# Performance work log

Hardware: AMD Instinct MI355X
Metric: run time of the kernel (lower is better)

The kernel has to match this reference:

```python
import jax, jax.numpy as jnp
import numpy as np
from jax import lax

K = 15            # k_neighbors
EPS = 1e-8
N, D = 8192, 512


def _knn(emb, k):
    # pairwise euclidean distances via gram trick (torch.cdist p=2 equivalent)
    sq = jnp.sum(emb * emb, axis=1)                      # [N]
    d2 = sq[:, None] + sq[None, :] - 2.0 * (emb @ emb.T)  # [N, N]
    d = jnp.where(d2 > 0, jnp.sqrt(jnp.maximum(d2, 1e-24)), 0.0)
    neg_d, idx = lax.top_k(-d, k + 1)                    # smallest k+1 (incl. self)
    return -neg_d[:, 1:], idx[:, 1:]                     # drop self: [N,k], [N,k]


def _local_density(knn_dists):
    return 1.0 / (knn_dists.mean(axis=1) + EPS)          # [N]


def _angular_signature(emb, knn_idx, k):
    nb = emb[knn_idx]                                    # [N, k, D] gather
    v = nb - emb[:, None, :]                             # [N, k, D]
    v = v / jnp.maximum(jnp.linalg.norm(v, axis=2, keepdims=True), 1e-12)
    cos = jnp.einsum('nkd,nld->nkl', v, v)               # [N, k, k]
    iu0, iu1 = np.triu_indices(k, 1)                     # static upper-triangle mask
    return cos[:, iu0, iu1]                              # [N, k*(k-1)/2]


def setup_inputs() -> dict:
    key = jax.random.key(0)
    k1, k2 = jax.random.split(key)
    embeddings = jax.random.normal(k1, (N, D), dtype=jnp.float32)
    ref_embeddings = jax.random.normal(k2, (N, D), dtype=jnp.float32)
    return {"embeddings": embeddings, "ref_embeddings": ref_embeddings}


def reference(embeddings, ref_embeddings):
    k = K
    # reference geometry is a detached buffer (set_reference under no_grad)
    ref = lax.stop_gradient(ref_embeddings)
    ref_dists, ref_idx = _knn(ref, k)
    ref_density = _local_density(ref_dists)
    ref_angular = _angular_signature(ref, ref_idx, k)

    curr_dists, curr_idx = _knn(embeddings, k)

    # 1) normalized distance-distribution loss
    curr_dn = curr_dists / (curr_dists.mean(axis=1, keepdims=True) + EPS)
    ref_dn = ref_dists / (ref_dists.mean(axis=1, keepdims=True) + EPS)
    total = jnp.mean((curr_dn - ref_dn) ** 2)

    # 2) density preservation loss (use_density=True)
    curr_density = _local_density(curr_dists)
    cden = curr_density / (curr_density.mean() + EPS)
    rden = ref_density / (ref_density.mean() + EPS)
    total = total + 0.5 * jnp.mean((cden - rden) ** 2)

    # 3) angular structure loss (use_angular=True)
    curr_angular = _angular_signature(embeddings, curr_idx, k)
    total = total + 0.5 * jnp.mean((curr_angular - ref_angular) ** 2)
    return total
```

## Files before the change

kernel.cpp:

```cpp
#include <hip/hip_runtime.h>

#define N 8192
#define D 512
#define KNN 15
#define SC 8
#define NC 16
#define SPLITS 8
#define NCAND 32
#define NPAIR 105
#define EPSF 1e-8f

#define INF __int_as_float(0x7f800000)

typedef __attribute__((ext_vector_type(4))) float f32x4;
typedef __attribute__((ext_vector_type(4))) unsigned u32x4;
typedef __attribute__((ext_vector_type(8))) short s16x8;
typedef __attribute__((ext_vector_type(8))) unsigned short u16x8;
typedef unsigned long long u64;

typedef const unsigned int __attribute__((address_space(1)))* gp_t;
typedef unsigned int __attribute__((address_space(3)))* lp_t;

__device__ __forceinline__ void gl_lds16(const void* g, void* l) {
  __builtin_amdgcn_global_load_lds((gp_t)g, (lp_t)l, 16, 0, 0);
}

__device__ __forceinline__ unsigned short bf16_rne(float x) {
  unsigned int u = __float_as_uint(x);
  return (unsigned short)((u + 0x7fffu + ((u >> 16) & 1u)) >> 16);
}

#define VMCNT4 asm volatile("s_waitcnt vmcnt(4)" ::: "memory")
#define VMCNT0 asm volatile("s_waitcnt vmcnt(0)" ::: "memory")
#define LGKM0  asm volatile("s_waitcnt lgkmcnt(0)" ::: "memory")
#define CFENCE asm volatile("" ::: "memory")

__global__ __launch_bounds__(256)
void k_prep(const float* __restrict__ A, const float* __restrict__ B,
            unsigned short* __restrict__ hi, float* __restrict__ sq)
{
  const int tid = threadIdx.x;
  const int lane = tid & 63;
  const int row = blockIdx.x * 4 + (tid >> 6);
  const float* src = (row < N) ? (A + (size_t)row * D)
                               : (B + (size_t)(row - N) * D);
  const float4* s4 = (const float4*)src + lane * 2;
  const float4 x0 = s4[0], x1 = s4[1];
  const float xs[8] = {x0.x, x0.y, x0.z, x0.w, x1.x, x1.y, x1.z, x1.w};
  u16x8 hv;
  float s = 0.f;
#pragma unroll
  for (int j = 0; j < 8; ++j) {
    hv[j] = bf16_rne(xs[j]);
    s = fmaf(xs[j], xs[j], s);
  }
  *(u16x8*)(hi + (size_t)row * D + lane * 8) = hv;
#pragma unroll
  for (int o = 32; o; o >>= 1) s += __shfl_xor(s, o);
  if (lane == 0) sq[row] = s;
}

__global__ __launch_bounds__(256, 4)
void k_knn1(const unsigned short* __restrict__ hi,
            const float* __restrict__ sqall,
            unsigned* __restrict__ pk)
{
  __shared__ __align__(16) char smem[40960];
  unsigned* DtU = (unsigned*)smem;
  unsigned* SK = (unsigned*)smem;

  const int tid = threadIdx.x;
  const int lane = tid & 63, w = tid >> 6;
  const int wr = w >> 1, wc = w & 1;
  const int fr = lane & 15, fq = lane >> 4;
  const int sgx = fq ^ ((fr >> 1) & 3);

  const int rb = blockIdx.x, split = blockIdx.y, which = blockIdx.z;
  const int row0 = rb * 128;
  const int c0 = split * 1024;
  const unsigned short* Hi = hi + (size_t)which * N * D;
  const float* sq = sqall + which * N;

  const int rr = tid >> 2, sseg = tid & 3;
  const int ssg = sseg ^ ((rr >> 1) & 3);
  const unsigned short* pAh = Hi + (size_t)(row0 + rr) * D + ssg * 8;
  const unsigned short* pBh = Hi + (size_t)(c0 + rr) * D + ssg * 8;

  auto stage = [&](int sel) {
    char* d = smem + (sel << 14) + (w << 10);
    gl_lds16(pAh, d);
    gl_lds16(pAh + 32768, d + 4096);
    gl_lds16(pBh, d + 8192);
    gl_lds16(pBh + 32768, d + 12288);
    pAh += 32; pBh += 32;
  };

  const int srow = tid >> 1, ssub = tid & 1;
  unsigned tv[SC];
#pragma unroll
  for (int j = 0; j < SC; ++j) tv[j] = 0xFFFFFFFFu;

  float sqr[4][4];
#pragma unroll
  for (int m = 0; m < 4; ++m)
#pragma unroll
    for (int j = 0; j < 4; ++j)
      sqr[m][j] = sq[row0 + wr * 64 + m * 16 + fq * 4 + j];

#pragma unroll 1
  for (int t = 0; t < 8; ++t) {
    const int ct = c0 + t * 128;
    float sqc[4];
#pragma unroll
    for (int n = 0; n < 4; ++n) sqc[n] = sq[ct + wc * 64 + n * 16 + fr];

    f32x4 acc[4][4];
#pragma unroll
    for (int m = 0; m < 4; ++m)
#pragma unroll
      for (int n = 0; n < 4; ++n) acc[m][n] = (f32x4){0.f, 0.f, 0.f, 0.f};

    stage(0);
    int cur = 0;
#pragma unroll 1
    for (int kt = 0; kt < 16; ++kt) {
      if (kt < 15) {
        stage(cur ^ 1);
        VMCNT4;
      } else {
        VMCNT0;
      }
      __builtin_amdgcn_s_barrier();
      CFENCE;

      const short* Sb = (const short*)(smem + (cur << 14));
      s16x8 ah[4], bh[4];
#pragma unroll
      for (int m = 0; m < 4; ++m)
        ah[m] = *(const s16x8*)(Sb + (wr * 64 + m * 16 + fr) * 32 + sgx * 8);
#pragma unroll
      for (int n = 0; n < 4; ++n)
        bh[n] = *(const s16x8*)(Sb + 4096 + (wc * 64 + n * 16 + fr) * 32 + sgx * 8);
#pragma unroll
      for (int m = 0; m < 4; ++m)
#pragma unroll
        for (int n = 0; n < 4; ++n)
          acc[m][n] = __builtin_amdgcn_mfma_f32_16x16x32_bf16(ah[m], bh[n], acc[m][n], 0, 0, 0);

      LGKM0;
      __builtin_amdgcn_s_barrier();
      CFENCE;
      cur ^= 1;
    }
    pAh -= 512; pBh += 65024;

#pragma unroll 1
    for (int h = 0; h < 2; ++h) {
      if (wc == h) {
#pragma unroll
        for (int m = 0; m < 4; ++m)
#pragma unroll
          for (int n = 0; n < 4; ++n) {
            const int cl = n * 16 + fr;
            const int gcol = ct + h * 64 + cl;
            const int rbase = wr * 64 + m * 16 + fq * 4;
#pragma unroll
            for (int j = 0; j < 4; ++j) {
              const float d2 = fmaf(-2.0f, acc[m][n][j], sqr[m][j] + sqc[n]);
              unsigned key = (__float_as_uint(fmaxf(d2, 0.f)) & ~8191u) | (unsigned)gcol;
              if (row0 + rbase + j == gcol) key = 0xFFFFFFFFu;
              DtU[(rbase + j) * 68 + cl] = key;
            }
          }
      }
      __syncthreads();
      {
        unsigned kth = tv[SC - 1];
#pragma unroll 1
        for (int g = 0; g < 8; ++g) {
          const u32x4 dv = *(const u32x4*)&DtU[srow * 68 + ssub * 32 + g * 4];
#pragma unroll
          for (int i = 0; i < 4; ++i) {
            unsigned key = dv[i];
            if (key < kth) {
#pragma unroll
              for (int j = 0; j < SC; ++j) {
                const unsigned lo = min(tv[j], key);
                key = max(tv[j], key);
                tv[j] = lo;
              }
              kth = tv[SC - 1];
            }
          }
        }
      }
      __syncthreads();
    }
  }

#pragma unroll
  for (int j = 0; j < SC; ++j) SK[srow * 16 + ssub * 8 + j] = tv[j];
  __syncthreads();
  if (tid < 128) {
    const int grow = row0 + tid;
    const size_t pb = (((size_t)which * SPLITS + split) * N + grow) * NC;
    int p0 = 0, p1 = 0;
#pragma unroll
    for (int j = 0; j < NC; ++j) {
      const unsigned a = (p0 < SC) ? SK[tid * 16 + p0] : 0xFFFFFFFFu;
      const unsigned b = (p1 < SC) ? SK[tid * 16 + 8 + p1] : 0xFFFFFFFFu;
      const bool ta = a <= b;
      pk[pb + j] = ta ? a : b;
      if (ta) ++p0; else ++p1;
    }
  }
}

__global__ __launch_bounds__(256)
void k_tail(const float* __restrict__ emb, const float* __restrict__ ref,
            const float* __restrict__ sqall, const unsigned* __restrict__ pk,
            float* __restrict__ dens, float* __restrict__ l1p,
            float* __restrict__ angp)
{
  __shared__ __align__(16) short Vb[16][520];
  __shared__ float Gp[4][256];
  __shared__ float G[256];
  __shared__ float invn[16];
  __shared__ float cref[NPAIR];
  __shared__ float red2[256];
  __shared__ int idxs[2][16];
  __shared__ float dls[2][16];

  const int i = blockIdx.x;
  const int tid = threadIdx.x;
  const int lane = tid & 63;
  const int w = tid >> 6;

  if (w < 2) {
    const int which = 1 - w;
    const float* E = which ? ref : emb;
    const float* sqm = sqall + which * N;

    const int sp = lane >> 3, jj = lane & 7;
    const size_t kb = (((size_t)which * SPLITS + sp) * N + i) * NC;
    unsigned v0 = pk[kb + jj];
    unsigned v1 = pk[kb + 8 + jj];

#pragma unroll
    for (int k = 2; k <= 128; k <<= 1) {
#pragma unroll
      for (int s = k >> 1; s > 0; s >>= 1) {
        if (s == 64) {
          const unsigned mn = min(v0, v1), mx = max(v0, v1);
          v0 = mn; v1 = mx;
        } else {
          const unsigned o0 = __shfl_xor(v0, s);
          const unsigned o1 = __shfl_xor(v1, s);
          const bool low = ((lane & s) == 0);
          const bool dir0 = ((lane & k) == 0);
          const bool dir1 = (((64 + lane) & k) == 0);
          const unsigned a0 = min(v0, o0), b0 = max(v0, o0);
          v0 = (low == dir0) ? a0 : b0;
          const unsigned a1 = min(v1, o1), b1 = max(v1, o1);
          v1 = (low == dir1) ? a1 : b1;
        }
      }
    }

    const float4* orow = (const float4*)(E + (size_t)i * D) + lane * 2;
    const float4 o0 = orow[0], o1 = orow[1];
    const float sqr_ = sqm[i];

    u64 mykey = ~0ull;
#pragma unroll 4
    for (int c = 0; c < NCAND; ++c) {
      const int cl = (int)(__shfl(v0, c) & 8191u);
      const float4* crow = (const float4*)(E + (size_t)cl * D) + lane * 2;
      const float4 c0 = crow[0], c1 = crow[1];
      float s = o0.x*c0.x + o0.y*c0.y + o0.z*c0.z + o0.w*c0.w
              + o1.x*c1.x + o1.y*c1.y + o1.z*c1.z + o1.w*c1.w;
#pragma unroll
      for (int o = 32; o; o >>= 1) s += __shfl_xor(s, o);
      float d2 = fmaf(-2.0f, s, sqr_ + sqm[cl]);
      d2 = fmaxf(d2, 0.0f);
      const u64 key = ((u64)__float_as_uint(d2) << 32) | (unsigned)cl;
      if (lane == c) mykey = key;
    }

#pragma unroll
    for (int k = 2; k <= 64; k <<= 1) {
#pragma unroll
      for (int j = k >> 1; j > 0; j >>= 1) {
        const u64 o = __shfl_xor(mykey, j);
        const bool up = ((lane & k) == 0);
        const bool lower = ((lane & j) == 0);
        const u64 mn = (mykey < o) ? mykey : o;
        const u64 mx = (mykey < o) ? o : mykey;
        mykey = (lower == up) ? mn : mx;
      }
    }

    if (lane < KNN) {
      const float d2v = __uint_as_float((unsigned)(mykey >> 32));
      dls[w][lane] = (d2v > 0.f) ? sqrtf(fmaxf(d2v, 1e-24f)) : 0.f;
      idxs[w][lane] = (int)(mykey & 0xffffffffu);
    }
  }
  __syncthreads();

  if (tid == 0) {
    float mr = 0.f, mc = 0.f;
#pragma unroll
    for (int j = 0; j < KNN; ++j) { mr += dls[0][j]; mc += dls[1][j]; }
    mr *= (1.0f / KNN); mc *= (1.0f / KNN);
    const float ir = 1.0f / (mr + EPSF);
    const float ic = 1.0f / (mc + EPSF);
    float s1 = 0.f;
#pragma unroll
    for (int j = 0; j < KNN; ++j) {
      const float t = dls[1][j] * ic - dls[0][j] * ir;
      s1 = fmaf(t, t, s1);
    }
    dens[i] = ic;
    dens[N + i] = ir;
    l1p[i] = s1;
  }
  __syncthreads();

  const int base = lane * 8;
  float acc = 0.f;

#pragma unroll 1
  for (int pass = 0; pass < 2; ++pass) {
    const float* E = pass ? emb : ref;

    const float4* er = (const float4*)(E + (size_t)i * D) + lane * 2;
    const float4 e0 = er[0], e1 = er[1];

#pragma unroll 1
    for (int j = w; j < 16; j += 4) {
      u16x8 hv;
      if (j < 15) {
        const float* src = E + (size_t)idxs[pass][j] * D;
        const float4 x0 = *(const float4*)(src + base);
        const float4 x1 = *(const float4*)(src + base + 4);
        const float dd[8] = {x0.x-e0.x, x0.y-e0.y, x0.z-e0.z, x0.w-e0.w,
                             x1.x-e1.x, x1.y-e1.y, x1.z-e1.z, x1.w-e1.w};
#pragma unroll
        for (int q = 0; q < 8; ++q) hv[q] = bf16_rne(dd[q]);
      } else {
#pragma unroll
        for (int q = 0; q < 8; ++q) hv[q] = 0;
      }
      *(u16x8*)&Vb[j][base] = hv;
    }
    __syncthreads();

    {
      const int r = lane & 15, fq = lane >> 4;
      f32x4 g = (f32x4){0.f, 0.f, 0.f, 0.f};
#pragma unroll
      for (int s = 0; s < 4; ++s) {
        const s16x8 f = *(const s16x8*)&Vb[r][w * 128 + s * 32 + fq * 8];
        g = __builtin_amdgcn_mfma_f32_16x16x32_bf16(f, f, g, 0, 0, 0);
      }
#pragma unroll
      for (int r2 = 0; r2 < 4; ++r2)
        Gp[w][(fq * 4 + r2) * 16 + r] = g[r2];
    }
    __syncthreads();

    G[tid] = Gp[0][tid] + Gp[1][tid] + Gp[2][tid] + Gp[3][tid];
    __syncthreads();
    if (tid < 16) invn[tid] = 1.0f / fmaxf(sqrtf(G[tid * 17]), 1e-12f);
    __syncthreads();

    if (tid < NPAIR) {
      int a = 0, q = tid, rem = KNN - 1;
      while (q >= rem) { q -= rem; ++a; --rem; }
      const int b = a + 1 + q;
      const float cosv = G[a * 16 + b] * invn[a] * invn[b];
      if (pass == 0) cref[tid] = cosv;
      else { const float dd = cosv - cref[tid]; acc = dd * dd; }
    }
    __syncthreads();
  }

  red2[tid] = acc;
  __syncthreads();
  for (int o = 128; o; o >>= 1) {
    if (tid < o) red2[tid] += red2[tid + o];
    __syncthreads();
  }
  if (tid == 0) angp[i] = red2[0];
}

__global__ __launch_bounds__(256)
void k_final(const float* __restrict__ l1p, const float* __restrict__ dens,
             const float* __restrict__ angp, float* __restrict__ out)
{
  __shared__ float red[256];
  const int t = threadIdx.x;

  float sc = 0.f, sr = 0.f;
  for (int n = t; n < N; n += 256) { sc += dens[n]; sr += dens[N + n]; }
  red[t] = sc; __syncthreads();
  for (int o = 128; o; o >>= 1) { if (t < o) red[t] += red[t + o]; __syncthreads(); }
  float scm = red[0]; __syncthreads();
  red[t] = sr; __syncthreads();
  for (int o = 128; o; o >>= 1) { if (t < o) red[t] += red[t + o]; __syncthreads(); }
  float srm = red[0]; __syncthreads();

  const float icm = 1.0f / (scm / (float)N + EPSF);
  const float irm = 1.0f / (srm / (float)N + EPSF);

  float l2 = 0.f;
  for (int n = t; n < N; n += 256) {
    const float dd = dens[n] * icm - dens[N + n] * irm;
    l2 = fmaf(dd, dd, l2);
  }
  red[t] = l2; __syncthreads();
  for (int o = 128; o; o >>= 1) { if (t < o) red[t] += red[t + o]; __syncthreads(); }
  const float l2sum = red[0]; __syncthreads();

  float l1 = 0.f;
  for (int n = t; n < N; n += 256) l1 += l1p[n];
  red[t] = l1; __syncthreads();
  for (int o = 128; o; o >>= 1) { if (t < o) red[t] += red[t + o]; __syncthreads(); }
  const float l1sum = red[0]; __syncthreads();

  float l3 = 0.f;
  for (int n = t; n < N; n += 256) l3 += angp[n];
  red[t] = l3; __syncthreads();
  for (int o = 128; o; o >>= 1) { if (t < o) red[t] += red[t + o]; __syncthreads(); }
  const float l3sum = red[0];

  if (t == 0) {
    out[0] = l1sum / (float)(N * KNN)
           + 0.5f * l2sum / (float)N
           + 0.5f * l3sum / (float)(N * NPAIR);
  }
}

extern "C" void kernel_launch(void* const* d_in, const int* in_sizes, int n_in,
                              void* d_out, int out_size, void* d_ws, size_t ws_size,
                              hipStream_t stream)
{
  const float* emb = (const float*)d_in[0];
  const float* ref = (const float*)d_in[1];
  float* out = (float*)d_out;
  char* ws = (char*)d_ws;

  const size_t off_sq   = 0;
  const size_t off_hi   = off_sq + (size_t)2 * N * 4;
  const size_t off_pk   = off_hi + (size_t)2 * N * D * 2;
  const size_t off_dens = off_pk + (size_t)2 * SPLITS * N * NC * 4;
  const size_t off_l1   = off_dens + (size_t)2 * N * 4;
  const size_t off_ang  = off_l1 + (size_t)N * 4;

  float* sq = (float*)(ws + off_sq);
  unsigned short* hi = (unsigned short*)(ws + off_hi);
  unsigned* pk = (unsigned*)(ws + off_pk);
  float* dens = (float*)(ws + off_dens);
  float* l1p = (float*)(ws + off_l1);
  float* angp = (float*)(ws + off_ang);

  k_prep<<<(2 * N) / 4, 256, 0, stream>>>(emb, ref, hi, sq);
  k_knn1<<<dim3(N / 128, SPLITS, 2), 256, 0, stream>>>(hi, sq, pk);
  k_tail<<<N, 256, 0, stream>>>(emb, ref, sq, pk, dens, l1p, angp);
  k_final<<<1, 256, 0, stream>>>(l1p, dens, angp, out);
}
```

Baseline: 367.2 us.

## Spread candidate rescoring and angular Gram work across all four waves

Candidate rescoring used to run on two waves, one per embedding set, with 32 candidates each. It now uses all four waves at 16 candidates each, sharing candidates and keys through LDS plus extra barriers. The two-pass angular Gram computation becomes a single pass: two waves build each set's difference matrix, and each wave runs 8 MFMAs over half of D. This removes a serial loop and several syncs, in exchange for more LDS and extra barriers around the merge.

```diff
diff --git a/kernel.cpp b/kernel.cpp
--- a/kernel.cpp
+++ b/kernel.cpp
@@ -222,14 +222,15 @@
             float* __restrict__ dens, float* __restrict__ l1p,
             float* __restrict__ angp)
 {
-  __shared__ __align__(16) short Vb[16][520];
+  __shared__ __align__(16) short Vb[2][16][520];
   __shared__ float Gp[4][256];
-  __shared__ float G[256];
-  __shared__ float invn[16];
-  __shared__ float cref[NPAIR];
-  __shared__ float red2[256];
+  __shared__ float G2[2][256];
+  __shared__ float invn[2][16];
+  __shared__ int cand[2][32];
+  __shared__ u64 kbuf[2][32];
   __shared__ int idxs[2][16];
   __shared__ float dls[2][16];
+  __shared__ float red2[256];
 
   const int i = blockIdx.x;
   const int tid = threadIdx.x;
@@ -238,14 +239,10 @@
 
   if (w < 2) {
     const int which = 1 - w;
-    const float* E = which ? ref : emb;
-    const float* sqm = sqall + which * N;
-
     const int sp = lane >> 3, jj = lane & 7;
     const size_t kb = (((size_t)which * SPLITS + sp) * N + i) * NC;
     unsigned v0 = pk[kb + jj];
     unsigned v1 = pk[kb + 8 + jj];
-
 #pragma unroll
     for (int k = 2; k <= 128; k <<= 1) {
 #pragma unroll
@@ -266,15 +263,24 @@
         }
       }
     }
+    if (lane < NCAND) cand[w][lane] = (int)(v0 & 8191u);
+  }
+  __syncthreads();
+
+  {
+    const int slot = w & 1, half = w >> 1;
+    const int which = 1 - slot;
+    const float* E = which ? ref : emb;
+    const float* sqm = sqall + which * N;
 
     const float4* orow = (const float4*)(E + (size_t)i * D) + lane * 2;
     const float4 o0 = orow[0], o1 = orow[1];
     const float sqr_ = sqm[i];
 
-    u64 mykey = ~0ull;
+    u64 myk = ~0ull;
 #pragma unroll 4
-    for (int c = 0; c < NCAND; ++c) {
-      const int cl = (int)(__shfl(v0, c) & 8191u);
+    for (int c = 0; c < 16; ++c) {
+      const int cl = cand[slot][half * 16 + c];
       const float4* crow = (const float4*)(E + (size_t)cl * D) + lane * 2;
       const float4 c0 = crow[0], c1 = crow[1];
       float s = o0.x*c0.x + o0.y*c0.y + o0.z*c0.z + o0.w*c0.w
@@ -284,9 +290,14 @@
       float d2 = fmaf(-2.0f, s, sqr_ + sqm[cl]);
       d2 = fmaxf(d2, 0.0f);
       const u64 key = ((u64)__float_as_uint(d2) << 32) | (unsigned)cl;
-      if (lane == c) mykey = key;
-    }
-
+      if (lane == c) myk = key;
+    }
+    if (lane < 16) kbuf[slot][half * 16 + lane] = myk;
+  }
+  __syncthreads();
+
+  if (w < 2) {
+    u64 mykey = (lane < NCAND) ? kbuf[w][lane] : ~0ull;
 #pragma unroll
     for (int k = 2; k <= 64; k <<= 1) {
 #pragma unroll
@@ -299,7 +310,6 @@
         mykey = (lower == up) ? mn : mx;
       }
     }
-
     if (lane < KNN) {
       const float d2v = __uint_as_float((unsigned)(mykey >> 32));
       dls[w][lane] = (d2v > 0.f) ? sqrtf(fmaxf(d2v, 1e-24f)) : 0.f;
@@ -325,23 +335,20 @@
     dens[N + i] = ir;
     l1p[i] = s1;
   }
-  __syncthreads();
-
-  const int base = lane * 8;
-  float acc = 0.f;
-
-#pragma unroll 1
-  for (int pass = 0; pass < 2; ++pass) {
-    const float* E = pass ? emb : ref;
+
+  {
+    const int p = w >> 1, w2 = w & 1;
+    const float* E = p ? emb : ref;
+    const int base = lane * 8;
 
     const float4* er = (const float4*)(E + (size_t)i * D) + lane * 2;
     const float4 e0 = er[0], e1 = er[1];
 
 #pragma unroll 1
-    for (int j = w; j < 16; j += 4) {
+    for (int j = w2; j < 16; j += 2) {
       u16x8 hv;
       if (j < 15) {
-        const float* src = E + (size_t)idxs[pass][j] * D;
+        const float* src = E + (size_t)idxs[p][j] * D;
         const float4 x0 = *(const float4*)(src + base);
         const float4 x1 = *(const float4*)(src + base + 4);
         const float dd[8] = {x0.x-e0.x, x0.y-e0.y, x0.z-e0.z, x0.w-e0.w,
@@ -352,38 +359,44 @@
 #pragma unroll
         for (int q = 0; q < 8; ++q) hv[q] = 0;
       }
-      *(u16x8*)&Vb[j][base] = hv;
-    }
-    __syncthreads();
-
-    {
-      const int r = lane & 15, fq = lane >> 4;
-      f32x4 g = (f32x4){0.f, 0.f, 0.f, 0.f};
-#pragma unroll
-      for (int s = 0; s < 4; ++s) {
-        const s16x8 f = *(const s16x8*)&Vb[r][w * 128 + s * 32 + fq * 8];
-        g = __builtin_amdgcn_mfma_f32_16x16x32_bf16(f, f, g, 0, 0, 0);
-      }
-#pragma unroll
-      for (int r2 = 0; r2 < 4; ++r2)
-        Gp[w][(fq * 4 + r2) * 16 + r] = g[r2];
-    }
-    __syncthreads();
-
-    G[tid] = Gp[0][tid] + Gp[1][tid] + Gp[2][tid] + Gp[3][tid];
-    __syncthreads();
-    if (tid < 16) invn[tid] = 1.0f / fmaxf(sqrtf(G[tid * 17]), 1e-12f);
-    __syncthreads();
-
-    if (tid < NPAIR) {
-      int a = 0, q = tid, rem = KNN - 1;
-      while (q >= rem) { q -= rem; ++a; --rem; }
-      const int b = a + 1 + q;
-      const float cosv = G[a * 16 + b] * invn[a] * invn[b];
-      if (pass == 0) cref[tid] = cosv;
-      else { const float dd = cosv - cref[tid]; acc = dd * dd; }
-    }
-    __syncthreads();
+      *(u16x8*)&Vb[p][j][base] = hv;
+    }
+  }
+  __syncthreads();
+
+  {
+    const int p = w >> 1, w2 = w & 1;
+    const int r = lane & 15, fq = lane >> 4;
+    f32x4 g = (f32x4){0.f, 0.f, 0.f, 0.f};
+#pragma unroll
+    for (int s = 0; s < 8; ++s) {
+      const s16x8 f = *(const s16x8*)&Vb[p][r][w2 * 256 + s * 32 + fq * 8];
+      g = __builtin_amdgcn_mfma_f32_16x16x32_bf16(f, f, g, 0, 0, 0);
+    }
+#pragma unroll
+    for (int r2 = 0; r2 < 4; ++r2)
+      Gp[w][(fq * 4 + r2) * 16 + r] = g[r2];
+  }
+  __syncthreads();
+
+  G2[0][tid] = Gp[0][tid] + Gp[1][tid];
+  G2[1][tid] = Gp[2][tid] + Gp[3][tid];
+  __syncthreads();
+  if (tid < 32) {
+    const int p = tid >> 4, r = tid & 15;
+    invn[p][r] = 1.0f / fmaxf(sqrtf(G2[p][r * 17]), 1e-12f);
+  }
+  __syncthreads();
+
+  float acc = 0.f;
+  if (tid < NPAIR) {
+    int a = 0, q = tid, rem = KNN - 1;
+    while (q >= rem) { q -= rem; ++a; --rem; }
+    const int b = a + 1 + q;
+    const float cos0 = G2[0][a * 16 + b] * invn[0][a] * invn[0][b];
+    const float cos1 = G2[1][a * 16 + b] * invn[1][a] * invn[1][b];
+    const float dd = cos1 - cos0;
+    acc = dd * dd;
   }
 
   red2[tid] = acc;
```

Result: slower. 388.5 us (+5.8%).
